# Performance work log

Measured on AMD Instinct MI355X. Metric: run time of the kernel, lower is better.

The kernel has to match this reference:

```python
import jax, jax.numpy as jnp
import numpy as np

N_NODES = 100000
N_EDGES = 625000
HIDDEN = 128
N_LAYERS = 4
NUM_GRAPHS = 512
INPUT_DIM = 28
EDGE_DIM = 4
OUT_DIM = 1


def setup_inputs() -> dict:
    key = jax.random.key(0)
    ks = jax.random.split(key, 16)
    x = jax.random.randint(ks[0], (N_NODES, 1), 0, INPUT_DIM)
    edge_index = jax.random.randint(ks[1], (2, N_EDGES), 0, N_NODES)
    edge_attr = jax.random.randint(ks[2], (N_EDGES,), 0, EDGE_DIM)
    batch = jnp.sort(jax.random.randint(ks[3], (N_NODES,), 0, NUM_GRAPHS))
    s = 1.0 / np.sqrt(HIDDEN)
    node_emb = jax.random.normal(ks[4], (INPUT_DIM, HIDDEN), jnp.float32)
    edge_emb = jax.random.normal(ks[5], (EDGE_DIM, HIDDEN), jnp.float32)
    conv_W1 = jax.random.normal(ks[6], (N_LAYERS, HIDDEN, HIDDEN), jnp.float32) * s
    conv_b1 = jnp.zeros((N_LAYERS, HIDDEN), jnp.float32)
    conv_W2 = jax.random.normal(ks[7], (N_LAYERS, HIDDEN, HIDDEN), jnp.float32) * s
    conv_b2 = jnp.zeros((N_LAYERS, HIDDEN), jnp.float32)
    mlp_W1 = jax.random.normal(ks[8], (HIDDEN, HIDDEN // 2), jnp.float32) * s
    mlp_b1 = jnp.zeros((HIDDEN // 2,), jnp.float32)
    mlp_W2 = jax.random.normal(ks[9], (HIDDEN // 2, HIDDEN // 4), jnp.float32) * (1.0 / np.sqrt(HIDDEN // 2))
    mlp_b2 = jnp.zeros((HIDDEN // 4,), jnp.float32)
    mlp_W3 = jax.random.normal(ks[10], (HIDDEN // 4, OUT_DIM), jnp.float32) * (1.0 / np.sqrt(HIDDEN // 4))
    mlp_b3 = jnp.zeros((OUT_DIM,), jnp.float32)
    return dict(x=x, edge_index=edge_index, edge_attr=edge_attr, batch=batch,
                node_emb=node_emb, edge_emb=edge_emb,
                conv_W1=conv_W1, conv_b1=conv_b1, conv_W2=conv_W2, conv_b2=conv_b2,
                mlp_W1=mlp_W1, mlp_b1=mlp_b1, mlp_W2=mlp_W2, mlp_b2=mlp_b2,
                mlp_W3=mlp_W3, mlp_b3=mlp_b3)


def reference(x, edge_index, edge_attr, batch, node_emb, edge_emb,
              conv_W1, conv_b1, conv_W2, conv_b2,
              mlp_W1, mlp_b1, mlp_W2, mlp_b2, mlp_W3, mlp_b3):
    h = node_emb[x[:, 0]]                    # [N, H] embedding lookup (x.squeeze(-1))
    _attr = edge_emb[edge_attr]              # computed in original forward but unused by GINConv
    src, dst = edge_index[0], edge_index[1]
    for l in range(N_LAYERS):
        # GINConv (eps=0): mlp((1+eps)*x + sum_{j->i} x_j)
        agg = jax.ops.segment_sum(h[src], dst, num_segments=N_NODES)  # [N, H]
        z = agg + h
        z = jax.nn.relu(z @ conv_W1[l] + conv_b1[l])
        h = z @ conv_W2[l] + conv_b2[l]
    g = jax.ops.segment_sum(h, batch, num_segments=NUM_GRAPHS)        # global_add_pool [G, H]
    g = jax.nn.relu(g @ mlp_W1 + mlp_b1)
    g = jax.nn.relu(g @ mlp_W2 + mlp_b2)
    return g @ mlp_W3 + mlp_b3               # [G, 1]
```

## Files before the change

### kernel.cpp

```cpp
#include <hip/hip_runtime.h>

#define N_NODES 100000
#define N_EDGES 625000
#define HIDDEN 128
#define NUM_GRAPHS 512
#define CAP 40

typedef unsigned int uint;
typedef unsigned short ushort;
typedef short v8s __attribute__((ext_vector_type(8)));
typedef float v16f __attribute__((ext_vector_type(16)));

__device__ __forceinline__ float b2f_lo(uint u) { return __uint_as_float(u << 16); }
__device__ __forceinline__ float b2f_hi(uint u) { return __uint_as_float(u & 0xffff0000u); }
__device__ __forceinline__ uint f2b(float f) {
  uint u = __float_as_uint(f);
  return (u + 0x7fffu + ((u >> 16) & 1u)) >> 16;
}

__global__ __launch_bounds__(256) void wtrans_k(const float* __restrict__ W1,
                                                const float* __restrict__ W2,
                                                ushort* __restrict__ Wt) {
  int mat = blockIdx.x;
  const float* W = ((mat & 1) ? W2 : W1) + (size_t)(mat >> 1) * 16384;
  ushort* o = Wt + (size_t)mat * 16384;
#pragma unroll
  for (int j = 0; j < 64; j++) {
    int idx = threadIdx.x + 256 * j;
    int k = idx >> 7, n = idx & 127;
    o[n * 128 + k] = (ushort)f2b(W[idx]);
  }
}

__global__ __launch_bounds__(256) void embed_k(const int* __restrict__ x,
                                               const float* __restrict__ emb,
                                               ushort* __restrict__ h) {
  int t = blockIdx.x * 256 + threadIdx.x;
  int n = t >> 4;
  if (n >= N_NODES) return;
  int c = t & 15;
  const float4* e = (const float4*)(emb + (size_t)x[n] * HIDDEN + c * 8);
  float4 a = e[0], b = e[1];
  uint4 o;
  o.x = f2b(a.x) | (f2b(a.y) << 16);
  o.y = f2b(a.z) | (f2b(a.w) << 16);
  o.z = f2b(b.x) | (f2b(b.y) << 16);
  o.w = f2b(b.z) | (f2b(b.w) << 16);
  ((uint4*)h)[t] = o;
}

__global__ __launch_bounds__(256) void build_k(const int* __restrict__ src,
                                               const int* __restrict__ dst,
                                               int* __restrict__ cursor,
                                               int* __restrict__ slots) {
  int e = blockIdx.x * 256 + threadIdx.x;
  if (e >= N_EDGES) return;
  int d = dst[e];
  int p = atomicAdd(&cursor[d], 1);
  if (p < CAP) slots[(size_t)d * CAP + p] = src[e];
}

__device__ __forceinline__ void stageW(const ushort* __restrict__ Wt, uint4* Wf, int tid) {
  const uint4* s = (const uint4*)Wt;
#pragma unroll
  for (int i = 0; i < 8; i++) {
    int idx = tid + 256 * i;
    int n = idx >> 4, j = idx & 15;
    Wf[(((n >> 5) * 8 + (j >> 1)) << 6) + ((j & 1) << 5) + (n & 31)] = s[idx];
  }
}

__device__ __forceinline__ void acc_row(const uint4* __restrict__ rowp, int khalf,
                                        float acc[8][8]) {
  uint4 u[8];
#pragma unroll
  for (int ks = 0; ks < 8; ks++) u[ks] = rowp[khalf + 2 * ks];
#pragma unroll
  for (int ks = 0; ks < 8; ks++) {
    acc[ks][0] += b2f_lo(u[ks].x); acc[ks][1] += b2f_hi(u[ks].x);
    acc[ks][2] += b2f_lo(u[ks].y); acc[ks][3] += b2f_hi(u[ks].y);
    acc[ks][4] += b2f_lo(u[ks].z); acc[ks][5] += b2f_hi(u[ks].z);
    acc[ks][6] += b2f_lo(u[ks].w); acc[ks][7] += b2f_hi(u[ks].w);
  }
}

__global__ __launch_bounds__(256, 2) void layer_k(const ushort* __restrict__ hin,
                                                  const int* __restrict__ cursor,
                                                  const int* __restrict__ slots,
                                                  const ushort* __restrict__ W1t,
                                                  const ushort* __restrict__ W2t,
                                                  const float* __restrict__ b1,
                                                  const float* __restrict__ b2,
                                                  ushort* __restrict__ hout) {
  __shared__ uint4 Wf[2048];
  __shared__ ushort zbuf[4 * 4096];

  int tid = threadIdx.x;
  int lane = tid & 63;
  int wv = tid >> 6;
  int l31 = lane & 31;
  int khalf = lane >> 5;
  int row = blockIdx.x * 128 + wv * 32 + l31;
  int arow = row < N_NODES ? row : N_NODES - 1;

  float bv1[4], bv2[4];
#pragma unroll
  for (int c = 0; c < 4; c++) { bv1[c] = b1[c * 32 + l31]; bv2[c] = b2[c * 32 + l31]; }

  stageW(W1t, Wf, tid);

  float acc[8][8];
#pragma unroll
  for (int ks = 0; ks < 8; ks++)
#pragma unroll
    for (int e = 0; e < 8; e++) acc[ks][e] = 0.f;

  const uint4* base = (const uint4*)hin;
  acc_row(base + (size_t)arow * 16, khalf, acc);
  int deg = (row < N_NODES) ? cursor[row] : 0;
  if (deg > CAP) deg = CAP;
  const int* sl = slots + (size_t)arow * CAP;
  int s = (deg > 0) ? sl[0] : 0;
  for (int j = 0; j < deg; j++) {
    int snext = (j + 1 < deg) ? sl[j + 1] : 0;
    acc_row(base + (size_t)s * 16, khalf, acc);
    s = snext;
  }

  union U { uint4 u; v8s s; };
  U afr[8];
#pragma unroll
  for (int ks = 0; ks < 8; ks++) {
    afr[ks].u.x = f2b(acc[ks][0]) | (f2b(acc[ks][1]) << 16);
    afr[ks].u.y = f2b(acc[ks][2]) | (f2b(acc[ks][3]) << 16);
    afr[ks].u.z = f2b(acc[ks][4]) | (f2b(acc[ks][5]) << 16);
    afr[ks].u.w = f2b(acc[ks][6]) | (f2b(acc[ks][7]) << 16);
  }

  __syncthreads();

  v16f acc1[4] = {};
#pragma unroll
  for (int c = 0; c < 4; c++)
#pragma unroll
    for (int ks = 0; ks < 8; ks++) {
      U b; b.u = Wf[((c * 8 + ks) << 6) + lane];
      acc1[c] = __builtin_amdgcn_mfma_f32_32x32x16_bf16(afr[ks].s, b.s, acc1[c], 0, 0, 0);
    }

  ushort* zb = zbuf + (wv << 12);
#pragma unroll
  for (int c = 0; c < 4; c++) {
    int col = c * 32 + l31;
    int zoff = ((col >> 4) << 9) + (((col >> 3) & 1) << 8) + (col & 7);
#pragma unroll
    for (int r = 0; r < 16; r++) {
      int orow = (r & 3) + 8 * (r >> 2) + 4 * khalf;
      float v = fmaxf(acc1[c][r] + bv1[c], 0.f);
      zb[zoff + orow * 8] = (ushort)f2b(v);
    }
  }

  __syncthreads();
  stageW(W2t, Wf, tid);
  __syncthreads();

  U az[8];
#pragma unroll
  for (int ks = 0; ks < 8; ks++)
    az[ks].u = *(const uint4*)(zb + ((ks << 6) + lane) * 8);

  v16f acc2[4] = {};
#pragma unroll
  for (int c = 0; c < 4; c++)
#pragma unroll
    for (int ks = 0; ks < 8; ks++) {
      U b; b.u = Wf[((c * 8 + ks) << 6) + lane];
      acc2[c] = __builtin_amdgcn_mfma_f32_32x32x16_bf16(az[ks].s, b.s, acc2[c], 0, 0, 0);
    }

  int rbase = blockIdx.x * 128 + wv * 32 + 4 * khalf;
#pragma unroll
  for (int c = 0; c < 4; c++) {
    int col = c * 32 + l31;
#pragma unroll
    for (int r = 0; r < 16; r++) {
      int orow = rbase + (r & 3) + 8 * (r >> 2);
      if (orow < N_NODES)
        hout[(size_t)orow * HIDDEN + col] = (ushort)f2b(acc2[c][r] + bv2[c]);
    }
  }
}

__global__ __launch_bounds__(256) void poolmlp_k(const ushort* __restrict__ h,
                                                 const int* __restrict__ batch,
                                                 const float* __restrict__ W1, const float* __restrict__ b1,
                                                 const float* __restrict__ W2, const float* __restrict__ b2,
                                                 const float* __restrict__ W3, const float* __restrict__ b3,
                                                 float* __restrict__ out) {
  __shared__ int se[2];
  __shared__ float red[16][16][8];
  __shared__ float gl[128];
  __shared__ float r2[64];
  __shared__ float r3[32];
  int gi = blockIdx.x, tid = threadIdx.x;
  if (tid < 2) {
    int target = gi + tid;
    int lo = 0, hi = N_NODES;
    while (lo < hi) {
      int mid = (lo + hi) >> 1;
      if (batch[mid] < target) lo = mid + 1; else hi = mid;
    }
    se[tid] = lo;
  }
  __syncthreads();
  int start = se[0], end = se[1];
  int cg = tid & 15, rg = tid >> 4;
  float acc[8] = {0.f, 0.f, 0.f, 0.f, 0.f, 0.f, 0.f, 0.f};
  for (int r = start + rg; r < end; r += 16) {
    uint4 v = ((const uint4*)h)[r * 16 + cg];
    acc[0] += b2f_lo(v.x); acc[1] += b2f_hi(v.x);
    acc[2] += b2f_lo(v.y); acc[3] += b2f_hi(v.y);
    acc[4] += b2f_lo(v.z); acc[5] += b2f_hi(v.z);
    acc[6] += b2f_lo(v.w); acc[7] += b2f_hi(v.w);
  }
#pragma unroll
  for (int j = 0; j < 8; j++) red[rg][cg][j] = acc[j];
  __syncthreads();
  if (rg == 0) {
    float s[8];
#pragma unroll
    for (int j = 0; j < 8; j++) s[j] = red[0][cg][j];
#pragma unroll
    for (int i = 1; i < 16; i++)
#pragma unroll
      for (int j = 0; j < 8; j++) s[j] += red[i][cg][j];
#pragma unroll
    for (int j = 0; j < 8; j++) gl[cg * 8 + j] = s[j];
  }
  __syncthreads();
  if (tid < 64) {
    float s = b1[tid];
    for (int k = 0; k < 128; k++) s = fmaf(gl[k], W1[k * 64 + tid], s);
    r2[tid] = fmaxf(s, 0.f);
  }
  __syncthreads();
  if (tid < 32) {
    float s2 = b2[tid];
    for (int k = 0; k < 64; k++) s2 = fmaf(r2[k], W2[k * 32 + tid], s2);
    r3[tid] = fmaxf(s2, 0.f);
  }
  __syncthreads();
  if (tid < 64) {
    float pv = (tid < 32) ? r3[tid] * W3[tid] : 0.f;
#pragma unroll
    for (int off = 32; off > 0; off >>= 1) pv += __shfl_down(pv, off);
    if (tid == 0) out[gi] = pv + b3[0];
  }
}

extern "C" void kernel_launch(void* const* d_in, const int* in_sizes, int n_in,
                              void* d_out, int out_size, void* d_ws, size_t ws_size,
                              hipStream_t stream) {
  const int* x = (const int*)d_in[0];
  const int* src = (const int*)d_in[1];
  const int* dst = src + N_EDGES;
  const int* batch = (const int*)d_in[3];
  const float* node_emb = (const float*)d_in[4];
  const float* cW1 = (const float*)d_in[6];
  const float* cb1 = (const float*)d_in[7];
  const float* cW2 = (const float*)d_in[8];
  const float* cb2 = (const float*)d_in[9];
  const float* mW1 = (const float*)d_in[10];
  const float* mb1 = (const float*)d_in[11];
  const float* mW2 = (const float*)d_in[12];
  const float* mb2 = (const float*)d_in[13];
  const float* mW3 = (const float*)d_in[14];
  const float* mb3 = (const float*)d_in[15];
  float* out = (float*)d_out;

  char* p = (char*)d_ws;
  const size_t HB = (size_t)N_NODES * HIDDEN * sizeof(ushort);
  ushort* h = (ushort*)p;      p += HB;
  ushort* t0 = (ushort*)p;     p += HB;
  ushort* Wtb = (ushort*)p;    p += (size_t)8 * 16384 * sizeof(ushort);
  int* cursor = (int*)p;       p += (size_t)N_NODES * sizeof(int);
  int* slots = (int*)p;        p += (size_t)N_NODES * CAP * sizeof(int);

  hipMemsetAsync(cursor, 0, (size_t)N_NODES * sizeof(int), stream);
  wtrans_k<<<8, 256, 0, stream>>>(cW1, cW2, Wtb);
  embed_k<<<(N_NODES * 16 + 255) / 256, 256, 0, stream>>>(x, node_emb, h);
  build_k<<<(N_EDGES + 255) / 256, 256, 0, stream>>>(src, dst, cursor, slots);

  const int grid = (N_NODES + 127) / 128;
  ushort* bufs[2] = {h, t0};
  for (int l = 0; l < 4; l++) {
    layer_k<<<grid, 256, 0, stream>>>(bufs[l & 1], cursor, slots,
                                      Wtb + (size_t)(2 * l) * 16384,
                                      Wtb + (size_t)(2 * l + 1) * 16384,
                                      cb1 + (size_t)l * HIDDEN,
                                      cb2 + (size_t)l * HIDDEN,
                                      bufs[(l & 1) ^ 1]);
  }
  poolmlp_k<<<NUM_GRAPHS, 256, 0, stream>>>(h, batch, mW1, mb1, mW2, mb2, mW3, mb3, out);
}
```

Baseline: 397.0 us.

## Keep GIN hidden activations in registers via transposed MFMA and direct-to-LDS weight loads

Swaps the operands of the first MFMA so each lane ends up holding a transposed slice of the hidden activation. A cross-half wave shuffle then rebuilds the A-fragments for the second matmul, which removes the per-wave zbuf LDS round trip. Weight staging now uses global_load_lds straight into LDS instead of loading through registers, the bias registers are dropped, and launch bounds go from 2 to 3 blocks per CU to hide more latency on the edge gather. The risks are register spills under the tighter budget and correct wait handling on the async LDS loads.

```diff
diff --git a/kernel.cpp b/kernel.cpp
--- a/kernel.cpp
+++ b/kernel.cpp
@@ -60,16 +60,6 @@
   if (p < CAP) slots[(size_t)d * CAP + p] = src[e];
 }
 
-__device__ __forceinline__ void stageW(const ushort* __restrict__ Wt, uint4* Wf, int tid) {
-  const uint4* s = (const uint4*)Wt;
-#pragma unroll
-  for (int i = 0; i < 8; i++) {
-    int idx = tid + 256 * i;
-    int n = idx >> 4, j = idx & 15;
-    Wf[(((n >> 5) * 8 + (j >> 1)) << 6) + ((j & 1) << 5) + (n & 31)] = s[idx];
-  }
-}
-
 __device__ __forceinline__ void acc_row(const uint4* __restrict__ rowp, int khalf,
                                         float acc[8][8]) {
   uint4 u[8];
@@ -84,7 +74,7 @@
   }
 }
 
-__global__ __launch_bounds__(256, 2) void layer_k(const ushort* __restrict__ hin,
+__global__ __launch_bounds__(256, 3) void layer_k(const ushort* __restrict__ hin,
                                                   const int* __restrict__ cursor,
                                                   const int* __restrict__ slots,
                                                   const ushort* __restrict__ W1t,
@@ -93,7 +83,6 @@
                                                   const float* __restrict__ b2,
                                                   ushort* __restrict__ hout) {
   __shared__ uint4 Wf[2048];
-  __shared__ ushort zbuf[4 * 4096];
 
   int tid = threadIdx.x;
   int lane = tid & 63;
@@ -103,11 +92,11 @@
   int row = blockIdx.x * 128 + wv * 32 + l31;
   int arow = row < N_NODES ? row : N_NODES - 1;
 
-  float bv1[4], bv2[4];
-#pragma unroll
-  for (int c = 0; c < 4; c++) { bv1[c] = b1[c * 32 + l31]; bv2[c] = b2[c * 32 + l31]; }
-
-  stageW(W1t, Wf, tid);
+#pragma unroll
+  for (int ks = 0; ks < 8; ks++) {
+    const uint4* g = (const uint4*)W1t + ((wv * 32 + l31) << 4) + 2 * ks + khalf;
+    __builtin_amdgcn_global_load_lds((const uint*)g, (uint*)(Wf + ((wv * 8 + ks) << 6)), 16, 0, 0);
+  }
 
   float acc[8][8];
 #pragma unroll
@@ -145,30 +134,53 @@
 #pragma unroll
     for (int ks = 0; ks < 8; ks++) {
       U b; b.u = Wf[((c * 8 + ks) << 6) + lane];
-      acc1[c] = __builtin_amdgcn_mfma_f32_32x32x16_bf16(afr[ks].s, b.s, acc1[c], 0, 0, 0);
+      acc1[c] = __builtin_amdgcn_mfma_f32_32x32x16_bf16(b.s, afr[ks].s, acc1[c], 0, 0, 0);
     }
 
-  ushort* zb = zbuf + (wv << 12);
-#pragma unroll
-  for (int c = 0; c < 4; c++) {
-    int col = c * 32 + l31;
-    int zoff = ((col >> 4) << 9) + (((col >> 3) & 1) << 8) + (col & 7);
-#pragma unroll
-    for (int r = 0; r < 16; r++) {
-      int orow = (r & 3) + 8 * (r >> 2) + 4 * khalf;
-      float v = fmaxf(acc1[c][r] + bv1[c], 0.f);
-      zb[zoff + orow * 8] = (ushort)f2b(v);
-    }
-  }
-
-  __syncthreads();
-  stageW(W2t, Wf, tid);
-  __syncthreads();
+  uint u[4][4][2];
+#pragma unroll
+  for (int c = 0; c < 4; c++)
+#pragma unroll
+    for (int b = 0; b < 4; b++)
+#pragma unroll
+      for (int ap = 0; ap < 2; ap++) {
+        int r0 = 2 * ap + 4 * b, r1 = r0 + 1;
+        float v0 = fmaxf(acc1[c][r0] + b1[c * 32 + 2 * ap + 8 * b + 4 * khalf], 0.f);
+        float v1 = fmaxf(acc1[c][r1] + b1[c * 32 + 2 * ap + 1 + 8 * b + 4 * khalf], 0.f);
+        u[c][b][ap] = f2b(v0) | (f2b(v1) << 16);
+      }
+
+  uint got[4][2][2];
+#pragma unroll
+  for (int c = 0; c < 4; c++)
+#pragma unroll
+    for (int bh = 0; bh < 2; bh++)
+#pragma unroll
+      for (int ap = 0; ap < 2; ap++) {
+        uint send = khalf ? u[c][2 * bh][ap] : u[c][2 * bh + 1][ap];
+        got[c][bh][ap] = __shfl_xor(send, 32, 64);
+      }
 
   U az[8];
 #pragma unroll
-  for (int ks = 0; ks < 8; ks++)
-    az[ks].u = *(const uint4*)(zb + ((ks << 6) + lane) * 8);
+  for (int ks = 0; ks < 8; ks++) {
+    uint o0 = khalf ? u[ks >> 1][2 * (ks & 1) + 1][0] : u[ks >> 1][2 * (ks & 1)][0];
+    uint o1 = khalf ? u[ks >> 1][2 * (ks & 1) + 1][1] : u[ks >> 1][2 * (ks & 1)][1];
+    uint g0 = got[ks >> 1][ks & 1][0];
+    uint g1 = got[ks >> 1][ks & 1][1];
+    az[ks].u.x = khalf ? g0 : o0;
+    az[ks].u.y = khalf ? g1 : o1;
+    az[ks].u.z = khalf ? o0 : g0;
+    az[ks].u.w = khalf ? o1 : g1;
+  }
+
+  __syncthreads();
+#pragma unroll
+  for (int ks = 0; ks < 8; ks++) {
+    const uint4* g = (const uint4*)W2t + ((wv * 32 + l31) << 4) + 2 * ks + khalf;
+    __builtin_amdgcn_global_load_lds((const uint*)g, (uint*)(Wf + ((wv * 8 + ks) << 6)), 16, 0, 0);
+  }
+  __syncthreads();
 
   v16f acc2[4] = {};
 #pragma unroll
@@ -187,7 +199,7 @@
     for (int r = 0; r < 16; r++) {
       int orow = rbase + (r & 3) + 8 * (r >> 2);
       if (orow < N_NODES)
-        hout[(size_t)orow * HIDDEN + col] = (ushort)f2b(acc2[c][r] + bv2[c]);
+        hout[(size_t)orow * HIDDEN + col] = (ushort)f2b(acc2[c][r] + b2[c * 32 + l31]);
     }
   }
 }
```

Measured after the change: 446.3 us. 1.12x slower.
